# Performance work log

Measured on AMD Instinct MI355X. Metric: run time of the kernel, lower is better.

## Reference

```python
import jax, jax.numpy as jnp
import numpy as np

B, L, HID, NH, HD = 1, 2304, 3072, 24, 128
IMG = 2048
MLP = 4 * HID  # 12288
EPS = 1e-6


def _layernorm(x):
    mu = jnp.mean(x, axis=-1, keepdims=True)
    var = jnp.mean(jnp.square(x - mu), axis=-1, keepdims=True)
    return (x - mu) * jax.lax.rsqrt(var + EPS)


def _rmsnorm(x, w):
    ms = jnp.mean(jnp.square(x), axis=-1, keepdims=True)
    return x * jax.lax.rsqrt(ms + EPS) * w


def _rope_interleaved(x, cos, sin):
    # x: [B, S, H, D]; cos/sin: [1, S, 1, D] with pairwise-equal values (mode=1, GPT-J)
    x1 = x[..., 0::2]
    x2 = x[..., 1::2]
    c = cos[..., 0::2]
    s = sin[..., 0::2]
    even = x1 * c - x2 * s
    odd = x1 * s + x2 * c
    return jnp.stack([even, odd], axis=-1).reshape(x.shape)


def setup_inputs() -> dict:
    key = jax.random.key(0)
    ks = jax.random.split(key, 10)
    scale_in = 1.0 / np.sqrt(HID)
    x = jax.random.normal(ks[0], (B, L, HID), jnp.float32)
    vec = jax.random.normal(ks[1], (B, HID), jnp.float32)
    # RoPE tables (interleaved layout: value repeated per pair)
    pos = jnp.arange(IMG, dtype=jnp.float32)
    inv_freq = 1.0 / (10000.0 ** (jnp.arange(HD // 2, dtype=jnp.float32) / (HD // 2)))
    ang = pos[:, None] * inv_freq[None, :]               # [IMG, HD/2]
    freqs_cos = jnp.repeat(jnp.cos(ang), 2, axis=-1).reshape(1, IMG, 1, HD)
    freqs_sin = jnp.repeat(jnp.sin(ang), 2, axis=-1).reshape(1, IMG, 1, HD)
    mod_w = jax.random.normal(ks[2], (HID, 3 * HID), jnp.float32) * scale_in
    mod_b = jnp.zeros((3 * HID,), jnp.float32)
    w1 = jax.random.normal(ks[3], (HID, 3 * HID + MLP), jnp.float32) * scale_in
    b1 = jnp.zeros((3 * HID + MLP,), jnp.float32)
    q_norm_w = jnp.ones((HD,), jnp.float32)
    k_norm_w = jnp.ones((HD,), jnp.float32)
    w2 = jax.random.normal(ks[4], (HID + MLP, HID), jnp.float32) * (1.0 / np.sqrt(HID + MLP))
    b2 = jnp.zeros((HID,), jnp.float32)
    return {
        'x': x, 'vec': vec, 'img_len': IMG,
        'freqs_cos': freqs_cos, 'freqs_sin': freqs_sin,
        'mod_w': mod_w, 'mod_b': mod_b, 'w1': w1, 'b1': b1,
        'q_norm_w': q_norm_w, 'k_norm_w': k_norm_w, 'w2': w2, 'b2': b2,
    }


def reference(x, vec, img_len, freqs_cos, freqs_sin, mod_w, mod_b, w1, b1,
              q_norm_w, k_norm_w, w2, b2):
    # modulation: SiLU(vec) -> Linear -> shift/scale/gate  [B, HID] each
    mod = jax.nn.silu(vec) @ mod_w + mod_b
    shift, scale, gate = jnp.split(mod, 3, axis=-1)
    x_mod = _layernorm(x) * (1.0 + scale[:, None, :]) + shift[:, None, :]

    # fused QKV + MLP projection
    proj = x_mod @ w1 + b1                                  # [B, L, 3*HID + MLP]
    qkv, mlp = proj[..., :3 * HID], proj[..., 3 * HID:]
    q, k, v = [t[:, :, 0] for t in [None]] if False else None, None, None
    qkv = qkv.reshape(B, L, 3, NH, HD)
    q, k, v = qkv[:, :, 0], qkv[:, :, 1], qkv[:, :, 2]      # [B, L, NH, HD]

    q = _rmsnorm(q, q_norm_w)
    k = _rmsnorm(k, k_norm_w)

    # RoPE only on image tokens
    q = jnp.concatenate([_rope_interleaved(q[:, :img_len], freqs_cos, freqs_sin), q[:, img_len:]], axis=1)
    k = jnp.concatenate([_rope_interleaved(k[:, :img_len], freqs_cos, freqs_sin), k[:, img_len:]], axis=1)

    # full (img+txt) bidirectional attention
    attn_scale = 1.0 / np.sqrt(HD)
    scores = jnp.einsum('blhd,bmhd->bhlm', q, k) * attn_scale
    probs = jax.nn.softmax(scores, axis=-1)
    attn = jnp.einsum('bhlm,bmhd->blhd', probs, v).reshape(B, L, NH * HD)

    # output fusion: [attn | gelu_tanh(mlp)] @ w2
    out = jnp.concatenate([attn, jax.nn.gelu(mlp, approximate=True)], axis=-1) @ w2 + b2
    return x + out * gate[:, None, :]
```

## Files before the change

### kernel.cpp

```cpp
#include <hip/hip_runtime.h>

#define L_SEQ 2304
#define HID_D 3072
#define NH_D 24
#define HD_D 128
#define N1_D 21504
#define QKVN 9216
#define K2_D 15360
#define EPS_V 1e-6f
#define ATTN_SC 0.08838834764831843f

typedef __bf16 bf16x8 __attribute__((ext_vector_type(8)));
typedef float f32x4 __attribute__((ext_vector_type(4)));
typedef unsigned int u32x4 __attribute__((ext_vector_type(4)));
typedef unsigned short u16x8 __attribute__((ext_vector_type(8)));
typedef unsigned short u16x4 __attribute__((ext_vector_type(4)));

#define WAITVM(N) asm volatile("s_waitcnt vmcnt(" #N ")" ::: "memory")
#define LGKM0 asm volatile("s_waitcnt lgkmcnt(0)" ::: "memory")
#define SB0 __builtin_amdgcn_sched_barrier(0)

__device__ __forceinline__ unsigned short f2bf(float f) {
  unsigned int u = __builtin_bit_cast(unsigned int, f);
  u += 0x7fffu + ((u >> 16) & 1u);
  return (unsigned short)(u >> 16);
}

__device__ __forceinline__ float gelu_f(float x) {
  float u = 0.7978845608028654f * (x + 0.044715f * x * x * x);
  float e = __expf(2.f * u);
  float th = 1.f - 2.f / (e + 1.f);
  return 0.5f * x * (1.f + th);
}

__device__ __forceinline__ void gload16(const void* g, void* l) {
  __builtin_amdgcn_global_load_lds(
      (const __attribute__((address_space(1))) unsigned int*)g,
      (__attribute__((address_space(3))) unsigned int*)l, 16, 0, 0);
}

__global__ __launch_bounds__(256) void mod_partial_kernel(
    const float* __restrict__ vec, const float* __restrict__ mod_w,
    float* __restrict__ partial) {
  __shared__ float s[384];
  const int t = threadIdx.x;
  const int kb = blockIdx.y;
  const int k0 = kb * 384;
  for (int p = t; p < 384; p += 256) {
    float v = vec[k0 + p];
    s[p] = v / (1.f + __expf(-v));
  }
  __syncthreads();
  const int n = blockIdx.x * 256 + t;
  float acc = 0.f;
  const float* wp = mod_w + (size_t)k0 * QKVN + n;
#pragma unroll 4
  for (int j = 0; j < 384; ++j) acc += s[j] * wp[(size_t)j * QKVN];
  partial[kb * QKVN + n] = acc;
}

__global__ __launch_bounds__(256) void mod_reduce_kernel(
    const float* __restrict__ partial, const float* __restrict__ mod_b,
    float* __restrict__ mod) {
  const int n = blockIdx.x * 256 + threadIdx.x;
  float acc = mod_b[n];
#pragma unroll
  for (int i = 0; i < 8; ++i) acc += partial[i * QKVN + n];
  mod[n] = acc;
}

__global__ __launch_bounds__(256) void ln_mod_kernel(
    const float* __restrict__ x, const float* __restrict__ mod,
    unsigned short* __restrict__ xmod) {
  const int row = blockIdx.x;
  const int t = threadIdx.x;
  const float* xr = x + (size_t)row * HID_D;
  float4 v[3];
  float sum = 0.f, sq = 0.f;
#pragma unroll
  for (int p = 0; p < 3; ++p) {
    v[p] = *(const float4*)&xr[p * 1024 + t * 4];
    sum += v[p].x + v[p].y + v[p].z + v[p].w;
    sq += v[p].x * v[p].x + v[p].y * v[p].y + v[p].z * v[p].z + v[p].w * v[p].w;
  }
#pragma unroll
  for (int o = 1; o < 64; o <<= 1) {
    sum += __shfl_xor(sum, o);
    sq += __shfl_xor(sq, o);
  }
  __shared__ float rs[8];
  const int w = t >> 6;
  if ((t & 63) == 0) { rs[w] = sum; rs[4 + w] = sq; }
  __syncthreads();
  sum = rs[0] + rs[1] + rs[2] + rs[3];
  sq = rs[4] + rs[5] + rs[6] + rs[7];
  const float mu = sum * (1.f / HID_D);
  const float var = sq * (1.f / HID_D) - mu * mu;
  const float rstd = rsqrtf(var + EPS_V);
#pragma unroll
  for (int p = 0; p < 3; ++p) {
    const int c = p * 1024 + t * 4;
    float4 sc = *(const float4*)&mod[3072 + c];
    float4 sh = *(const float4*)&mod[c];
    u16x4 o4;
    o4[0] = f2bf((v[p].x - mu) * rstd * (1.f + sc.x) + sh.x);
    o4[1] = f2bf((v[p].y - mu) * rstd * (1.f + sc.y) + sh.y);
    o4[2] = f2bf((v[p].z - mu) * rstd * (1.f + sc.z) + sh.z);
    o4[3] = f2bf((v[p].w - mu) * rstd * (1.f + sc.w) + sh.w);
    *(u16x4*)&xmod[(size_t)row * HID_D + c] = o4;
  }
}

__global__ __launch_bounds__(256) void convert_transpose_kernel(
    const float* __restrict__ src, unsigned short* __restrict__ dst,
    const int K, const int N) {
  __shared__ unsigned short lt[64][72];
  const int t = threadIdx.x;
  const int n0 = blockIdx.x * 64;
  const int k0 = blockIdx.y * 64;
  const int kr = t >> 4;
  const int n4 = (t & 15) * 4;
#pragma unroll
  for (int p = 0; p < 4; ++p) {
    const int k = kr + p * 16;
    float4 v = *(const float4*)&src[(size_t)(k0 + k) * N + n0 + n4];
    lt[n4 + 0][k] = f2bf(v.x);
    lt[n4 + 1][k] = f2bf(v.y);
    lt[n4 + 2][k] = f2bf(v.z);
    lt[n4 + 3][k] = f2bf(v.w);
  }
  __syncthreads();
  const int nr = t >> 2;
  const int kc = (t & 3) * 16;
  u16x8 a = *(const u16x8*)&lt[nr][kc];
  u16x8 b = *(const u16x8*)&lt[nr][kc + 8];
  unsigned short* dp = &dst[(size_t)(n0 + nr) * K + k0 + kc];
  *(u16x8*)dp = a;
  *(u16x8*)(dp + 8) = b;
}

template <int BM>
__device__ __forceinline__ void gemm8_core(
    const unsigned short* __restrict__ A, const int lda,
    const unsigned short* __restrict__ B, const int ldb,
    const int m0, const int n0, const int nit, char* lds, f32x4 (*acc)[4]) {
  constexpr int AREG = (BM == 256) ? 16384 : 8192;
  constexpr int ABUF = 2 * AREG;
  constexpr int BOFF = 2 * ABUF;
  constexpr int BREG = 16384;
  constexpr int BBUF = 32768;
  constexpr int AROWS = (BM == 256) ? 128 : 64;
  constexpr int AI = (BM == 256) ? 2 : 1;
  constexpr int MF = (BM == 256) ? 4 : 2;
  constexpr int QM = (BM == 256) ? 64 : 32;

  const int t = threadIdx.x;
  const int lane = t & 63;
  const int w = t >> 6;
  const int g = lane >> 4;
  const int c = lane & 15;
  const int sr8 = lane >> 3;
  const int scol = ((lane & 7) ^ sr8) * 8;
  const int arg = w >> 2;
  const int brg = (w & 3) >> 1;
  const int bbase = (w & 1) * 64;

  auto stageA = [&](int buf, int rg, int kt) {
#pragma unroll
    for (int i = 0; i < AI; ++i)
      gload16(A + (size_t)(m0 + rg * AROWS + i * 64 + w * 8 + sr8) * lda +
                  kt * 64 + scol,
              lds + buf * ABUF + rg * AREG + i * 8192 + w * 1024);
  };
  auto stageB = [&](int buf, int rg, int kt) {
#pragma unroll
    for (int i = 0; i < 2; ++i)
      gload16(B + (size_t)(n0 + rg * 128 + i * 64 + w * 8 + sr8) * ldb +
                  kt * 64 + scol,
              lds + BOFF + buf * BBUF + rg * BREG + i * 8192 + w * 1024);
  };

  bf16x8 af[2 * MF], bq0[4], bq1[4];
  auto ldA = [&](int buf, int qm) {
    const char* ab = lds + buf * ABUF + arg * AREG;
#pragma unroll
    for (int i = 0; i < MF; ++i) {
      const int lr = qm * QM + i * 16 + c;
#pragma unroll
      for (int kk = 0; kk < 2; ++kk)
        af[i * 2 + kk] =
            *(const bf16x8*)(ab + lr * 128 + (((kk * 4 + g) ^ (c & 7)) << 4));
    }
  };
  auto ldB = [&](int buf, int qn, bf16x8* bq) {
    const char* bb = lds + BOFF + buf * BBUF + brg * BREG;
#pragma unroll
    for (int i = 0; i < 2; ++i) {
      const int lr = bbase + qn * 32 + i * 16 + c;
#pragma unroll
      for (int kk = 0; kk < 2; ++kk)
        bq[i * 2 + kk] =
            *(const bf16x8*)(bb + lr * 128 + (((kk * 4 + g) ^ (c & 7)) << 4));
    }
  };
  auto domf = [&](int qm, int qn, const bf16x8* bq) {
#pragma unroll
    for (int i = 0; i < MF; ++i)
#pragma unroll
      for (int n = 0; n < 2; ++n)
#pragma unroll
        for (int kk = 0; kk < 2; ++kk)
          acc[qm * MF + i][qn * 2 + n] = __builtin_amdgcn_mfma_f32_16x16x32_bf16(
              af[i * 2 + kk], bq[n * 2 + kk], acc[qm * MF + i][qn * 2 + n], 0, 0, 0);
  };
  auto MID = [&] {
    SB0;
    __builtin_amdgcn_s_barrier();
    LGKM0;
    SB0;
    __builtin_amdgcn_s_setprio(1);
  };
  auto END = [&] {
    __builtin_amdgcn_s_setprio(0);
    SB0;
    __builtin_amdgcn_s_barrier();
  };

  stageB(0, 0, 0); stageA(0, 0, 0); stageB(0, 1, 0); stageA(0, 1, 0);
  stageB(1, 0, 1); stageA(1, 0, 1);
  if constexpr (BM == 256) WAITVM(4); else WAITVM(3);
  __builtin_amdgcn_s_barrier();

  for (int j = 0; j < nit; ++j) {
    const int ta = 2 * j;
    const bool nl = (j + 1 < nit);
    ldA(0, 0); ldB(0, 0, bq0);
    stageB(1, 1, ta + 1);
    MID(); domf(0, 0, bq0); END();
    ldB(0, 1, bq1);
    stageA(1, 1, ta + 1);
    MID(); domf(0, 1, bq1); END();
    ldA(0, 1);
    if (nl) stageB(0, 0, ta + 2);
    MID(); domf(1, 1, bq1); END();
    if (nl) stageA(0, 0, ta + 2);
    MID(); domf(1, 0, bq0);
    __builtin_amdgcn_s_setprio(0); SB0;
    if (nl) { if constexpr (BM == 256) WAITVM(4); else WAITVM(3); }
    else WAITVM(0);
    __builtin_amdgcn_s_barrier();
    ldA(1, 0); ldB(1, 0, bq0);
    if (nl) stageB(0, 1, ta + 2);
    MID(); domf(0, 0, bq0); END();
    ldB(1, 1, bq1);
    if (nl) stageA(0, 1, ta + 2);
    MID(); domf(0, 1, bq1); END();
    ldA(1, 1);
    if (nl) stageB(1, 0, ta + 3);
    MID(); domf(1, 1, bq1); END();
    if (nl) stageA(1, 0, ta + 3);
    MID(); domf(1, 0, bq0);
    __builtin_amdgcn_s_setprio(0); SB0;
    if (nl) { if constexpr (BM == 256) WAITVM(4); else WAITVM(3); }
    __builtin_amdgcn_s_barrier();
  }
}

__global__ __launch_bounds__(512, 2) void gemm1_kernel(
    const unsigned short* __restrict__ xmod, const unsigned short* __restrict__ w1t,
    const float* __restrict__ b1, float* __restrict__ qkv,
    unsigned short* __restrict__ hbuf) {
  __shared__ __align__(16) char smem[131072];
  f32x4 acc[8][4];
  const f32x4 zero = {0.f, 0.f, 0.f, 0.f};
#pragma unroll
  for (int i = 0; i < 8; ++i)
#pragma unroll
    for (int j = 0; j < 4; ++j) acc[i][j] = zero;
  const int orig = blockIdx.x;
  const int xcd = orig & 7;
  const int wgid = (xcd < 4 ? xcd * 95 : 380 + (xcd - 4) * 94) + (orig >> 3);
  const int m0 = (wgid % 9) * 256;
  const int n0 = (wgid / 9) * 256;
  gemm8_core<256>(xmod, HID_D, w1t, HID_D, m0, n0, 24, smem, acc);
  const int lane = threadIdx.x & 63;
  const int g = lane >> 4, c = lane & 15;
  const int w = threadIdx.x >> 6;
  const int wm = (w >> 2) * 128, wn = (w & 3) * 64;
  const bool is_mlp = (n0 >= QKVN);
#pragma unroll
  for (int mf = 0; mf < 8; ++mf)
#pragma unroll
    for (int nf = 0; nf < 4; ++nf)
#pragma unroll
      for (int j = 0; j < 4; ++j) {
        const int row = m0 + wm + mf * 16 + g * 4 + j;
        const int col = n0 + wn + nf * 16 + c;
        const float v = acc[mf][nf][j] + b1[col];
        if (!is_mlp) {
          qkv[(size_t)row * QKVN + col] = v;
        } else {
          hbuf[(size_t)row * K2_D + HID_D + (col - QKVN)] = f2bf(gelu_f(v));
        }
      }
}

__global__ __launch_bounds__(512, 2) void gemm2_kernel(
    const unsigned short* __restrict__ hbuf, const unsigned short* __restrict__ w2t,
    const float* __restrict__ b2, const float* __restrict__ x,
    const float* __restrict__ mod, float* __restrict__ out) {
  __shared__ __align__(16) char smem[98304];
  f32x4 acc[4][4];
  const f32x4 zero = {0.f, 0.f, 0.f, 0.f};
#pragma unroll
  for (int i = 0; i < 4; ++i)
#pragma unroll
    for (int j = 0; j < 4; ++j) acc[i][j] = zero;
  const int orig = blockIdx.x;
  const int wgid = (orig & 7) * 27 + (orig >> 3);
  const int m0 = (wgid % 18) * 128;
  const int n0 = (wgid / 18) * 256;
  gemm8_core<128>(hbuf, K2_D, w2t, K2_D, m0, n0, 120, smem, acc);
  const int lane = threadIdx.x & 63;
  const int g = lane >> 4, c = lane & 15;
  const int w = threadIdx.x >> 6;
  const int wm = (w >> 2) * 64, wn = (w & 3) * 64;
#pragma unroll
  for (int mf = 0; mf < 4; ++mf)
#pragma unroll
    for (int nf = 0; nf < 4; ++nf)
#pragma unroll
      for (int j = 0; j < 4; ++j) {
        const int row = m0 + wm + mf * 16 + g * 4 + j;
        const int col = n0 + wn + nf * 16 + c;
        const float v = acc[mf][nf][j] + b2[col];
        out[(size_t)row * HID_D + col] =
            x[(size_t)row * HID_D + col] + v * mod[6144 + col];
      }
}

__global__ __launch_bounds__(256) void qk_norm_rope_kernel(
    const float* __restrict__ qkv, const float* __restrict__ qw,
    const float* __restrict__ kw, const float* __restrict__ fc,
    const float* __restrict__ fs, const int* __restrict__ img_len_p,
    unsigned short* __restrict__ qr, unsigned short* __restrict__ kr) {
  const int l = blockIdx.x;
  const int t = threadIdx.x;
  const int wv = t >> 6;
  const int lane = t & 63;
  const int img = *img_len_p;
  const bool do_rope = (l < img);
  float cc = 1.f, ss = 0.f;
  if (do_rope) {
    cc = fc[l * HD_D + 2 * lane];
    ss = fs[l * HD_D + 2 * lane];
  }
  const float qw0 = qw[2 * lane], qw1 = qw[2 * lane + 1];
  const float kw0 = kw[2 * lane], kw1 = kw[2 * lane + 1];
#pragma unroll
  for (int hh = 0; hh < 6; ++hh) {
    const int h = hh * 4 + wv;
    {
      float2 q2 = *(const float2*)&qkv[(size_t)l * QKVN + h * HD_D + 2 * lane];
      float sq = q2.x * q2.x + q2.y * q2.y;
#pragma unroll
      for (int o = 1; o < 64; o <<= 1) sq += __shfl_xor(sq, o);
      const float r = rsqrtf(sq * (1.f / HD_D) + EPS_V);
      float a = q2.x * r * qw0, b = q2.y * r * qw1;
      float e = a, od = b;
      if (do_rope) { e = a * cc - b * ss; od = a * ss + b * cc; }
      e *= ATTN_SC; od *= ATTN_SC;
      unsigned int pk = (unsigned)f2bf(e) | ((unsigned)f2bf(od) << 16);
      *(unsigned int*)&qr[((size_t)h * L_SEQ + l) * HD_D + 2 * lane] = pk;
    }
    {
      float2 k2 = *(const float2*)&qkv[(size_t)l * QKVN + HID_D + h * HD_D + 2 * lane];
      float sq = k2.x * k2.x + k2.y * k2.y;
#pragma unroll
      for (int o = 1; o < 64; o <<= 1) sq += __shfl_xor(sq, o);
      const float r = rsqrtf(sq * (1.f / HD_D) + EPS_V);
      float a = k2.x * r * kw0, b = k2.y * r * kw1;
      float e = a, od = b;
      if (do_rope) { e = a * cc - b * ss; od = a * ss + b * cc; }
      unsigned int pk = (unsigned)f2bf(e) | ((unsigned)f2bf(od) << 16);
      *(unsigned int*)&kr[((size_t)h * L_SEQ + l) * HD_D + 2 * lane] = pk;
    }
  }
}

__global__ __launch_bounds__(256) void v_transpose_kernel(
    const float* __restrict__ qkv, unsigned short* __restrict__ vT) {
  __shared__ unsigned short lv[128 * 64];
  const int h = blockIdx.y;
  const int l0 = blockIdx.x * 64;
  const int t = threadIdx.x;
#pragma unroll
  for (int p = 0; p < 8; ++p) {
    const int idx = p * 256 + t;
    const int l = idx >> 5;
    const int d4 = (idx & 31) * 4;
    float4 v = *(const float4*)&qkv[(size_t)(l0 + l) * QKVN + 2 * HID_D + h * HD_D + d4];
    const unsigned sw = (unsigned)(((d4 >> 2) & 7) << 4);
    *(unsigned short*)((char*)lv + (((d4 + 0) * 128 + 2 * l) ^ sw)) = f2bf(v.x);
    *(unsigned short*)((char*)lv + (((d4 + 1) * 128 + 2 * l) ^ sw)) = f2bf(v.y);
    *(unsigned short*)((char*)lv + (((d4 + 2) * 128 + 2 * l) ^ sw)) = f2bf(v.z);
    *(unsigned short*)((char*)lv + (((d4 + 3) * 128 + 2 * l) ^ sw)) = f2bf(v.w);
  }
  __syncthreads();
  const int d = t >> 1;
  const int half = t & 1;
  const unsigned swr = (unsigned)(((d >> 2) & 7) << 4);
#pragma unroll
  for (int j2 = 0; j2 < 4; ++j2) {
    u32x4 v = *(const u32x4*)((const char*)lv + ((d * 128 + half * 64 + j2 * 16) ^ swr));
    *(u32x4*)&vT[(size_t)(h * HD_D + d) * L_SEQ + l0 + half * 32 + j2 * 8] = v;
  }
}

__global__ __launch_bounds__(256) void attn_kernel(
    const unsigned short* __restrict__ qr, const unsigned short* __restrict__ kr,
    const unsigned short* __restrict__ vT, unsigned short* __restrict__ hbuf) {
  __shared__ unsigned short lds_k[64 * 128];
  __shared__ unsigned short lds_v[128 * 64];
  __shared__ unsigned short lds_p[4 * 16 * 64];
  const int hidx = blockIdx.y;
  const int l0 = blockIdx.x * 64;
  const int t = threadIdx.x;
  const int lane = t & 63;
  const int w = t >> 6;
  const int g = lane >> 4;
  const int c = lane & 15;

  bf16x8 qa[4];
  {
    const unsigned short* qrow = qr + ((size_t)hidx * L_SEQ + l0 + w * 16 + c) * HD_D;
#pragma unroll
    for (int ks = 0; ks < 4; ++ks)
      qa[ks] = *(const bf16x8*)&qrow[ks * 32 + g * 8];
  }
  f32x4 acc[8];
  const f32x4 zero = {0.f, 0.f, 0.f, 0.f};
#pragma unroll
  for (int i = 0; i < 8; ++i) acc[i] = zero;
  float m_r[4] = {-1e30f, -1e30f, -1e30f, -1e30f};
  float l_r[4] = {0.f, 0.f, 0.f, 0.f};

  for (int kv0 = 0; kv0 < L_SEQ; kv0 += 64) {
    __syncthreads();
#pragma unroll
    for (int p = 0; p < 4; ++p) {
      const int idx = p * 256 + t;
      const int r = idx >> 4, ch = idx & 15;
      u32x4 v = *(const u32x4*)&kr[((size_t)hidx * L_SEQ + kv0 + r) * HD_D + ch * 8];
      *(u32x4*)((char*)lds_k + ((r * 256 + ch * 16) ^ ((r & 7) << 4))) = v;
    }
#pragma unroll
    for (int p = 0; p < 4; ++p) {
      const int idx = p * 256 + t;
      const int d_ = idx >> 3, ch = idx & 7;
      u32x4 v = *(const u32x4*)&vT[(size_t)(hidx * HD_D + d_) * L_SEQ + kv0 + ch * 8];
      *(u32x4*)((char*)lds_v + ((d_ * 128 + ch * 16) ^ ((d_ & 7) << 4))) = v;
    }
    __syncthreads();
    f32x4 s[4];
#pragma unroll
    for (int cf = 0; cf < 4; ++cf) s[cf] = zero;
#pragma unroll
    for (int ks = 0; ks < 4; ++ks) {
      const int kb = (ks * 32 + g * 8) * 2;
#pragma unroll
      for (int cf = 0; cf < 4; ++cf) {
        const int kvr = cf * 16 + c;
        bf16x8 kf = *(const bf16x8*)((const char*)lds_k + ((kvr * 256 + kb) ^ ((kvr & 7) << 4)));
        s[cf] = __builtin_amdgcn_mfma_f32_16x16x32_bf16(qa[ks], kf, s[cf], 0, 0, 0);
      }
    }
    float pv[4][4];
    float alpha[4];
#pragma unroll
    for (int r = 0; r < 4; ++r) {
      float mx = fmaxf(fmaxf(s[0][r], s[1][r]), fmaxf(s[2][r], s[3][r]));
      mx = fmaxf(mx, __shfl_xor(mx, 1));
      mx = fmaxf(mx, __shfl_xor(mx, 2));
      mx = fmaxf(mx, __shfl_xor(mx, 4));
      mx = fmaxf(mx, __shfl_xor(mx, 8));
      const float mnew = fmaxf(m_r[r], mx);
      alpha[r] = __expf(m_r[r] - mnew);
      float rsum = 0.f;
#pragma unroll
      for (int cf = 0; cf < 4; ++cf) {
        const float p_ = __expf(s[cf][r] - mnew);
        pv[cf][r] = p_;
        rsum += p_;
      }
      rsum += __shfl_xor(rsum, 1);
      rsum += __shfl_xor(rsum, 2);
      rsum += __shfl_xor(rsum, 4);
      rsum += __shfl_xor(rsum, 8);
      l_r[r] = l_r[r] * alpha[r] + rsum;
      m_r[r] = mnew;
    }
#pragma unroll
    for (int of = 0; of < 8; ++of)
#pragma unroll
      for (int r = 0; r < 4; ++r) acc[of][r] *= alpha[r];
#pragma unroll
    for (int cf = 0; cf < 4; ++cf)
#pragma unroll
      for (int r = 0; r < 4; ++r) {
        const int row = g * 4 + r;
        const int col = cf * 16 + c;
        *(unsigned short*)((char*)lds_p +
                           ((w * 2048 + row * 128 + col * 2) ^ ((row & 7) << 4))) =
            f2bf(pv[cf][r]);
      }
    asm volatile("s_waitcnt lgkmcnt(0)" ::: "memory");
    __builtin_amdgcn_sched_barrier(0);
#pragma unroll
    for (int ks = 0; ks < 2; ++ks) {
      bf16x8 pa = *(const bf16x8*)((const char*)lds_p +
                                   ((w * 2048 + c * 128 + (ks * 32 + g * 8) * 2) ^
                                    ((c & 7) << 4)));
#pragma unroll
      for (int of = 0; of < 8; ++of) {
        const int dcol = of * 16 + c;
        bf16x8 vb = *(const bf16x8*)((const char*)lds_v +
                                     ((dcol * 128 + (ks * 32 + g * 8) * 2) ^
                                      ((dcol & 7) << 4)));
        acc[of] = __builtin_amdgcn_mfma_f32_16x16x32_bf16(pa, vb, acc[of], 0, 0, 0);
      }
    }
  }
#pragma unroll
  for (int of = 0; of < 8; ++of)
#pragma unroll
    for (int r = 0; r < 4; ++r) {
      const int row = l0 + w * 16 + g * 4 + r;
      const int col = hidx * HD_D + of * 16 + c;
      hbuf[(size_t)row * K2_D + col] = f2bf(acc[of][r] / l_r[r]);
    }
}

extern "C" void kernel_launch(void* const* d_in, const int* in_sizes, int n_in,
                              void* d_out, int out_size, void* d_ws, size_t ws_size,
                              hipStream_t stream) {
  (void)in_sizes; (void)n_in; (void)out_size; (void)ws_size;
  const float* x = (const float*)d_in[0];
  const float* vec = (const float*)d_in[1];
  const int* img_len = (const int*)d_in[2];
  const float* fc = (const float*)d_in[3];
  const float* fs = (const float*)d_in[4];
  const float* mod_w = (const float*)d_in[5];
  const float* mod_b = (const float*)d_in[6];
  const float* w1 = (const float*)d_in[7];
  const float* b1 = (const float*)d_in[8];
  const float* qw = (const float*)d_in[9];
  const float* kw = (const float*)d_in[10];
  const float* w2 = (const float*)d_in[11];
  const float* b2 = (const float*)d_in[12];
  float* out = (float*)d_out;

  char* wsb = (char*)d_ws;
  float* mod = (float*)(wsb + 0);
  float* partial = (float*)(wsb + 36864);
  unsigned short* xmod = (unsigned short*)(wsb + 331776);
  float* qkv = (float*)(wsb + 14487552);
  unsigned short* hbuf = (unsigned short*)(wsb + 99422208);
  unsigned short* qr = (unsigned short*)(wsb + 170201088);
  unsigned short* kr = (unsigned short*)(wsb + 184356864);
  unsigned short* vT = (unsigned short*)(wsb + 198512640);
  unsigned short* wt = (unsigned short*)(wsb + 212668416);

  mod_partial_kernel<<<dim3(36, 8), 256, 0, stream>>>(vec, mod_w, partial);
  mod_reduce_kernel<<<36, 256, 0, stream>>>(partial, mod_b, mod);
  ln_mod_kernel<<<2304, 256, 0, stream>>>(x, mod, xmod);
  convert_transpose_kernel<<<dim3(N1_D / 64, HID_D / 64), 256, 0, stream>>>(
      w1, wt, HID_D, N1_D);
  gemm1_kernel<<<756, 512, 0, stream>>>(xmod, wt, b1, qkv, hbuf);
  convert_transpose_kernel<<<dim3(HID_D / 64, K2_D / 64), 256, 0, stream>>>(
      w2, wt, K2_D, HID_D);
  qk_norm_rope_kernel<<<2304, 256, 0, stream>>>(qkv, qw, kw, fc, fs, img_len, qr, kr);
  v_transpose_kernel<<<dim3(36, 24), 256, 0, stream>>>(qkv, vT);
  attn_kernel<<<dim3(36, 24), 256, 0, stream>>>(qr, kr, vT, hbuf);
  gemm2_kernel<<<216, 512, 0, stream>>>(hbuf, wt, b2, x, mod, out);
}
```

Measured before the change: 935.7 us.

## Store QKV intermediate as bf16 and triple-buffer the second GEMM pipeline

The fp32 QKV buffer written by the first GEMM is replaced with bf16, which halves its write and read traffic in the QK-norm/RoPE and V-transpose kernels. The second GEMM switches from a double-buffered core to a new three-stage LDS pipeline (144KB shared memory, 80 iterations of three k-tiles) so that more global loads are in flight during MFMA work. The pipeline adds LDS pressure, which may lower occupancy. Rounding Q/K/V to bf16 before the norm adds a small precision loss.

```diff
diff --git a/kernel.cpp b/kernel.cpp
--- a/kernel.cpp
+++ b/kernel.cpp
@@ -24,6 +24,9 @@
   unsigned int u = __builtin_bit_cast(unsigned int, f);
   u += 0x7fffu + ((u >> 16) & 1u);
   return (unsigned short)(u >> 16);
+}
+__device__ __forceinline__ float bf2f(unsigned short u) {
+  return __builtin_bit_cast(float, (unsigned int)u << 16);
 }
 
 __device__ __forceinline__ float gelu_f(float x) {
@@ -266,9 +269,124 @@
   }
 }
 
+__device__ __forceinline__ void gemm6_core(
+    const unsigned short* __restrict__ A, const int lda,
+    const unsigned short* __restrict__ B, const int ldb,
+    const int m0, const int n0, const int nit3, char* lds, f32x4 (*acc)[4]) {
+  const int t = threadIdx.x;
+  const int lane = t & 63;
+  const int w = t >> 6;
+  const int g = lane >> 4;
+  const int c = lane & 15;
+  const int sr8 = lane >> 3;
+  const int scol = ((lane & 7) ^ sr8) * 8;
+  const int arg = w >> 2;
+  const int brg = (w & 3) >> 1;
+  const int bbase = (w & 1) * 64;
+
+  auto stageA = [&](int buf, int kt) {
+#pragma unroll
+    for (int rg = 0; rg < 2; ++rg)
+      gload16(A + (size_t)(m0 + rg * 64 + w * 8 + sr8) * lda + kt * 64 + scol,
+              lds + buf * 16384 + rg * 8192 + w * 1024);
+  };
+  auto stageB = [&](int buf, int rg, int kt) {
+#pragma unroll
+    for (int i = 0; i < 2; ++i)
+      gload16(B + (size_t)(n0 + rg * 128 + i * 64 + w * 8 + sr8) * ldb +
+                  kt * 64 + scol,
+              lds + 49152 + buf * 32768 + rg * 16384 + i * 8192 + w * 1024);
+  };
+
+  bf16x8 af[8], bq[8];
+  auto ldA = [&](int buf) {
+    const char* ab = lds + buf * 16384 + arg * 8192;
+#pragma unroll
+    for (int i = 0; i < 4; ++i) {
+      const int lr = i * 16 + c;
+#pragma unroll
+      for (int kk = 0; kk < 2; ++kk)
+        af[i * 2 + kk] =
+            *(const bf16x8*)(ab + lr * 128 + (((kk * 4 + g) ^ (c & 7)) << 4));
+    }
+  };
+  auto ldB = [&](int buf, int half) {
+    const char* bb = lds + 49152 + buf * 32768 + brg * 16384;
+#pragma unroll
+    for (int i = 0; i < 2; ++i) {
+      const int lr = bbase + (half * 2 + i) * 16 + c;
+#pragma unroll
+      for (int kk = 0; kk < 2; ++kk)
+        bq[half * 4 + i * 2 + kk] =
+            *(const bf16x8*)(bb + lr * 128 + (((kk * 4 + g) ^ (c & 7)) << 4));
+    }
+  };
+  auto domf = [&](int half) {
+#pragma unroll
+    for (int i = 0; i < 4; ++i)
+#pragma unroll
+      for (int n = 0; n < 2; ++n)
+#pragma unroll
+        for (int kk = 0; kk < 2; ++kk)
+          acc[i][half * 2 + n] = __builtin_amdgcn_mfma_f32_16x16x32_bf16(
+              af[i * 2 + kk], bq[half * 4 + n * 2 + kk], acc[i][half * 2 + n],
+              0, 0, 0);
+  };
+  auto MID = [&] {
+    SB0;
+    __builtin_amdgcn_s_barrier();
+    LGKM0;
+    SB0;
+    __builtin_amdgcn_s_setprio(1);
+  };
+  auto END = [&] {
+    __builtin_amdgcn_s_setprio(0);
+    SB0;
+    __builtin_amdgcn_s_barrier();
+  };
+
+  stageA(0, 0); stageB(0, 0, 0); stageB(0, 1, 0);
+  stageA(1, 1); stageB(1, 0, 1); stageB(1, 1, 1);
+  stageA(2, 2);
+  WAITVM(8);
+  __builtin_amdgcn_s_barrier();
+
+  for (int j = 0; j < nit3; ++j) {
+    const int T = 3 * j;
+    const bool nl = (j + 1 < nit3);
+    ldA(0); ldB(0, 0);
+    stageB(2, 0, T + 2); stageB(2, 1, T + 2);
+    MID(); domf(0); END();
+    ldB(0, 1);
+    if (nl) stageA(0, T + 3);
+    MID(); domf(1);
+    __builtin_amdgcn_s_setprio(0); SB0;
+    if (nl) WAITVM(8); else WAITVM(6);
+    __builtin_amdgcn_s_barrier();
+    ldA(1); ldB(1, 0);
+    if (nl) stageB(0, 0, T + 3);
+    MID(); domf(0); END();
+    ldB(1, 1);
+    if (nl) { stageB(0, 1, T + 3); stageA(1, T + 4); }
+    MID(); domf(1);
+    __builtin_amdgcn_s_setprio(0); SB0;
+    if (nl) WAITVM(8); else WAITVM(0);
+    __builtin_amdgcn_s_barrier();
+    ldA(2); ldB(2, 0);
+    if (nl) { stageB(1, 0, T + 4); stageB(1, 1, T + 4); }
+    MID(); domf(0); END();
+    ldB(2, 1);
+    if (nl) stageA(2, T + 5);
+    MID(); domf(1);
+    __builtin_amdgcn_s_setprio(0); SB0;
+    if (nl) WAITVM(8);
+    __builtin_amdgcn_s_barrier();
+  }
+}
+
 __global__ __launch_bounds__(512, 2) void gemm1_kernel(
     const unsigned short* __restrict__ xmod, const unsigned short* __restrict__ w1t,
-    const float* __restrict__ b1, float* __restrict__ qkv,
+    const float* __restrict__ b1, unsigned short* __restrict__ qkv,
     unsigned short* __restrict__ hbuf) {
   __shared__ __align__(16) char smem[131072];
   f32x4 acc[8][4];
@@ -298,7 +416,7 @@
         const int col = n0 + wn + nf * 16 + c;
         const float v = acc[mf][nf][j] + b1[col];
         if (!is_mlp) {
-          qkv[(size_t)row * QKVN + col] = v;
+          qkv[(size_t)row * QKVN + col] = f2bf(v);
         } else {
           hbuf[(size_t)row * K2_D + HID_D + (col - QKVN)] = f2bf(gelu_f(v));
         }
@@ -309,7 +427,7 @@
     const unsigned short* __restrict__ hbuf, const unsigned short* __restrict__ w2t,
     const float* __restrict__ b2, const float* __restrict__ x,
     const float* __restrict__ mod, float* __restrict__ out) {
-  __shared__ __align__(16) char smem[98304];
+  __shared__ __align__(16) char smem[147456];
   f32x4 acc[4][4];
   const f32x4 zero = {0.f, 0.f, 0.f, 0.f};
 #pragma unroll
@@ -320,7 +438,7 @@
   const int wgid = (orig & 7) * 27 + (orig >> 3);
   const int m0 = (wgid % 18) * 128;
   const int n0 = (wgid / 18) * 256;
-  gemm8_core<128>(hbuf, K2_D, w2t, K2_D, m0, n0, 120, smem, acc);
+  gemm6_core(hbuf, K2_D, w2t, K2_D, m0, n0, 80, smem, acc);
   const int lane = threadIdx.x & 63;
   const int g = lane >> 4, c = lane & 15;
   const int w = threadIdx.x >> 6;
@@ -340,7 +458,7 @@
 }
 
 __global__ __launch_bounds__(256) void qk_norm_rope_kernel(
-    const float* __restrict__ qkv, const float* __restrict__ qw,
+    const unsigned short* __restrict__ qkv, const float* __restrict__ qw,
     const float* __restrict__ kw, const float* __restrict__ fc,
     const float* __restrict__ fs, const int* __restrict__ img_len_p,
     unsigned short* __restrict__ qr, unsigned short* __restrict__ kr) {
@@ -361,12 +479,14 @@
   for (int hh = 0; hh < 6; ++hh) {
     const int h = hh * 4 + wv;
     {
-      float2 q2 = *(const float2*)&qkv[(size_t)l * QKVN + h * HD_D + 2 * lane];
-      float sq = q2.x * q2.x + q2.y * q2.y;
+      unsigned int pq = *(const unsigned int*)&qkv[(size_t)l * QKVN + h * HD_D + 2 * lane];
+      float q0 = bf2f((unsigned short)(pq & 0xffff));
+      float q1 = bf2f((unsigned short)(pq >> 16));
+      float sq = q0 * q0 + q1 * q1;
 #pragma unroll
       for (int o = 1; o < 64; o <<= 1) sq += __shfl_xor(sq, o);
       const float r = rsqrtf(sq * (1.f / HD_D) + EPS_V);
-      float a = q2.x * r * qw0, b = q2.y * r * qw1;
+      float a = q0 * r * qw0, b = q1 * r * qw1;
       float e = a, od = b;
       if (do_rope) { e = a * cc - b * ss; od = a * ss + b * cc; }
       e *= ATTN_SC; od *= ATTN_SC;
@@ -374,12 +494,14 @@
       *(unsigned int*)&qr[((size_t)h * L_SEQ + l) * HD_D + 2 * lane] = pk;
     }
     {
-      float2 k2 = *(const float2*)&qkv[(size_t)l * QKVN + HID_D + h * HD_D + 2 * lane];
-      float sq = k2.x * k2.x + k2.y * k2.y;
+      unsigned int pkk = *(const unsigned int*)&qkv[(size_t)l * QKVN + HID_D + h * HD_D + 2 * lane];
+      float k0 = bf2f((unsigned short)(pkk & 0xffff));
+      float k1 = bf2f((unsigned short)(pkk >> 16));
+      float sq = k0 * k0 + k1 * k1;
 #pragma unroll
       for (int o = 1; o < 64; o <<= 1) sq += __shfl_xor(sq, o);
       const float r = rsqrtf(sq * (1.f / HD_D) + EPS_V);
-      float a = k2.x * r * kw0, b = k2.y * r * kw1;
+      float a = k0 * r * kw0, b = k1 * r * kw1;
       float e = a, od = b;
       if (do_rope) { e = a * cc - b * ss; od = a * ss + b * cc; }
       unsigned int pk = (unsigned)f2bf(e) | ((unsigned)f2bf(od) << 16);
@@ -389,22 +511,23 @@
 }
 
 __global__ __launch_bounds__(256) void v_transpose_kernel(
-    const float* __restrict__ qkv, unsigned short* __restrict__ vT) {
+    const unsigned short* __restrict__ qkv, unsigned short* __restrict__ vT) {
   __shared__ unsigned short lv[128 * 64];
   const int h = blockIdx.y;
   const int l0 = blockIdx.x * 64;
   const int t = threadIdx.x;
 #pragma unroll
-  for (int p = 0; p < 8; ++p) {
+  for (int p = 0; p < 4; ++p) {
     const int idx = p * 256 + t;
-    const int l = idx >> 5;
-    const int d4 = (idx & 31) * 4;
-    float4 v = *(const float4*)&qkv[(size_t)(l0 + l) * QKVN + 2 * HID_D + h * HD_D + d4];
-    const unsigned sw = (unsigned)(((d4 >> 2) & 7) << 4);
-    *(unsigned short*)((char*)lv + (((d4 + 0) * 128 + 2 * l) ^ sw)) = f2bf(v.x);
-    *(unsigned short*)((char*)lv + (((d4 + 1) * 128 + 2 * l) ^ sw)) = f2bf(v.y);
-    *(unsigned short*)((char*)lv + (((d4 + 2) * 128 + 2 * l) ^ sw)) = f2bf(v.z);
-    *(unsigned short*)((char*)lv + (((d4 + 3) * 128 + 2 * l) ^ sw)) = f2bf(v.w);
+    const int l = idx >> 4;
+    const int d8 = (idx & 15) * 8;
+    u16x8 v = *(const u16x8*)&qkv[(size_t)(l0 + l) * QKVN + 2 * HID_D + h * HD_D + d8];
+#pragma unroll
+    for (int e = 0; e < 8; ++e) {
+      const int d = d8 + e;
+      const unsigned sw = (unsigned)(((d >> 2) & 7) << 4);
+      *(unsigned short*)((char*)lv + (((unsigned)d * 128 + 2 * l) ^ sw)) = v[e];
+    }
   }
   __syncthreads();
   const int d = t >> 1;
@@ -564,7 +687,7 @@
   float* mod = (float*)(wsb + 0);
   float* partial = (float*)(wsb + 36864);
   unsigned short* xmod = (unsigned short*)(wsb + 331776);
-  float* qkv = (float*)(wsb + 14487552);
+  unsigned short* qkv = (unsigned short*)(wsb + 14487552);
   unsigned short* hbuf = (unsigned short*)(wsb + 99422208);
   unsigned short* qr = (unsigned short*)(wsb + 170201088);
   unsigned short* kr = (unsigned short*)(wsb + 184356864);
```

Result: slower. 966.9 us (+3.3%).

## Store QKV intermediate in bf16 and register-prefetch next attention K/V tile

Applied to the files above, without the earlier changes.

The gemm1 epilogue now writes the QKV projection as bf16 instead of fp32, and the qk-norm/rope and V-transpose kernels read bf16, which halves that intermediate's write and read traffic. The attention kernel loads the next K/V tile into registers while the current tile is being computed, overlapping global loads with MFMA work at the cost of extra registers. The final normalization uses a reciprocal multiply instead of a divide. Rounding QKV to bf16 before the RMS norm adds a small amount of precision loss.

```diff
diff --git a/kernel.cpp b/kernel.cpp
--- a/kernel.cpp
+++ b/kernel.cpp
@@ -24,6 +24,9 @@
   unsigned int u = __builtin_bit_cast(unsigned int, f);
   u += 0x7fffu + ((u >> 16) & 1u);
   return (unsigned short)(u >> 16);
+}
+__device__ __forceinline__ float bf2f(unsigned short u) {
+  return __builtin_bit_cast(float, (unsigned int)u << 16);
 }
 
 __device__ __forceinline__ float gelu_f(float x) {
@@ -268,7 +271,7 @@
 
 __global__ __launch_bounds__(512, 2) void gemm1_kernel(
     const unsigned short* __restrict__ xmod, const unsigned short* __restrict__ w1t,
-    const float* __restrict__ b1, float* __restrict__ qkv,
+    const float* __restrict__ b1, unsigned short* __restrict__ qkv,
     unsigned short* __restrict__ hbuf) {
   __shared__ __align__(16) char smem[131072];
   f32x4 acc[8][4];
@@ -298,7 +301,7 @@
         const int col = n0 + wn + nf * 16 + c;
         const float v = acc[mf][nf][j] + b1[col];
         if (!is_mlp) {
-          qkv[(size_t)row * QKVN + col] = v;
+          qkv[(size_t)row * QKVN + col] = f2bf(v);
         } else {
           hbuf[(size_t)row * K2_D + HID_D + (col - QKVN)] = f2bf(gelu_f(v));
         }
@@ -340,7 +343,7 @@
 }
 
 __global__ __launch_bounds__(256) void qk_norm_rope_kernel(
-    const float* __restrict__ qkv, const float* __restrict__ qw,
+    const unsigned short* __restrict__ qkv, const float* __restrict__ qw,
     const float* __restrict__ kw, const float* __restrict__ fc,
     const float* __restrict__ fs, const int* __restrict__ img_len_p,
     unsigned short* __restrict__ qr, unsigned short* __restrict__ kr) {
@@ -361,12 +364,14 @@
   for (int hh = 0; hh < 6; ++hh) {
     const int h = hh * 4 + wv;
     {
-      float2 q2 = *(const float2*)&qkv[(size_t)l * QKVN + h * HD_D + 2 * lane];
-      float sq = q2.x * q2.x + q2.y * q2.y;
+      unsigned int pq = *(const unsigned int*)&qkv[(size_t)l * QKVN + h * HD_D + 2 * lane];
+      float q0 = bf2f((unsigned short)(pq & 0xffff));
+      float q1 = bf2f((unsigned short)(pq >> 16));
+      float sq = q0 * q0 + q1 * q1;
 #pragma unroll
       for (int o = 1; o < 64; o <<= 1) sq += __shfl_xor(sq, o);
       const float r = rsqrtf(sq * (1.f / HD_D) + EPS_V);
-      float a = q2.x * r * qw0, b = q2.y * r * qw1;
+      float a = q0 * r * qw0, b = q1 * r * qw1;
       float e = a, od = b;
       if (do_rope) { e = a * cc - b * ss; od = a * ss + b * cc; }
       e *= ATTN_SC; od *= ATTN_SC;
@@ -374,12 +379,14 @@
       *(unsigned int*)&qr[((size_t)h * L_SEQ + l) * HD_D + 2 * lane] = pk;
     }
     {
-      float2 k2 = *(const float2*)&qkv[(size_t)l * QKVN + HID_D + h * HD_D + 2 * lane];
-      float sq = k2.x * k2.x + k2.y * k2.y;
+      unsigned int pkk = *(const unsigned int*)&qkv[(size_t)l * QKVN + HID_D + h * HD_D + 2 * lane];
+      float k0 = bf2f((unsigned short)(pkk & 0xffff));
+      float k1 = bf2f((unsigned short)(pkk >> 16));
+      float sq = k0 * k0 + k1 * k1;
 #pragma unroll
       for (int o = 1; o < 64; o <<= 1) sq += __shfl_xor(sq, o);
       const float r = rsqrtf(sq * (1.f / HD_D) + EPS_V);
-      float a = k2.x * r * kw0, b = k2.y * r * kw1;
+      float a = k0 * r * kw0, b = k1 * r * kw1;
       float e = a, od = b;
       if (do_rope) { e = a * cc - b * ss; od = a * ss + b * cc; }
       unsigned int pk = (unsigned)f2bf(e) | ((unsigned)f2bf(od) << 16);
@@ -389,22 +396,23 @@
 }
 
 __global__ __launch_bounds__(256) void v_transpose_kernel(
-    const float* __restrict__ qkv, unsigned short* __restrict__ vT) {
+    const unsigned short* __restrict__ qkv, unsigned short* __restrict__ vT) {
   __shared__ unsigned short lv[128 * 64];
   const int h = blockIdx.y;
   const int l0 = blockIdx.x * 64;
   const int t = threadIdx.x;
 #pragma unroll
-  for (int p = 0; p < 8; ++p) {
+  for (int p = 0; p < 4; ++p) {
     const int idx = p * 256 + t;
-    const int l = idx >> 5;
-    const int d4 = (idx & 31) * 4;
-    float4 v = *(const float4*)&qkv[(size_t)(l0 + l) * QKVN + 2 * HID_D + h * HD_D + d4];
-    const unsigned sw = (unsigned)(((d4 >> 2) & 7) << 4);
-    *(unsigned short*)((char*)lv + (((d4 + 0) * 128 + 2 * l) ^ sw)) = f2bf(v.x);
-    *(unsigned short*)((char*)lv + (((d4 + 1) * 128 + 2 * l) ^ sw)) = f2bf(v.y);
-    *(unsigned short*)((char*)lv + (((d4 + 2) * 128 + 2 * l) ^ sw)) = f2bf(v.z);
-    *(unsigned short*)((char*)lv + (((d4 + 3) * 128 + 2 * l) ^ sw)) = f2bf(v.w);
+    const int l = idx >> 4;
+    const int d8 = (idx & 15) * 8;
+    u16x8 v = *(const u16x8*)&qkv[(size_t)(l0 + l) * QKVN + 2 * HID_D + h * HD_D + d8];
+#pragma unroll
+    for (int e = 0; e < 8; ++e) {
+      const int d = d8 + e;
+      const unsigned sw = (unsigned)(((d >> 2) & 7) << 4);
+      *(unsigned short*)((char*)lv + (((unsigned)d * 128 + 2 * l) ^ sw)) = v[e];
+    }
   }
   __syncthreads();
   const int d = t >> 1;
@@ -445,23 +453,39 @@
   float m_r[4] = {-1e30f, -1e30f, -1e30f, -1e30f};
   float l_r[4] = {0.f, 0.f, 0.f, 0.f};
 
-  for (int kv0 = 0; kv0 < L_SEQ; kv0 += 64) {
-    __syncthreads();
+  u32x4 kreg[4], vreg[4];
+  auto load_tile = [&](int kv0) {
 #pragma unroll
     for (int p = 0; p < 4; ++p) {
       const int idx = p * 256 + t;
       const int r = idx >> 4, ch = idx & 15;
-      u32x4 v = *(const u32x4*)&kr[((size_t)hidx * L_SEQ + kv0 + r) * HD_D + ch * 8];
-      *(u32x4*)((char*)lds_k + ((r * 256 + ch * 16) ^ ((r & 7) << 4))) = v;
+      kreg[p] = *(const u32x4*)&kr[((size_t)hidx * L_SEQ + kv0 + r) * HD_D + ch * 8];
     }
 #pragma unroll
     for (int p = 0; p < 4; ++p) {
       const int idx = p * 256 + t;
       const int d_ = idx >> 3, ch = idx & 7;
-      u32x4 v = *(const u32x4*)&vT[(size_t)(hidx * HD_D + d_) * L_SEQ + kv0 + ch * 8];
-      *(u32x4*)((char*)lds_v + ((d_ * 128 + ch * 16) ^ ((d_ & 7) << 4))) = v;
-    }
+      vreg[p] = *(const u32x4*)&vT[(size_t)(hidx * HD_D + d_) * L_SEQ + kv0 + ch * 8];
+    }
+  };
+  load_tile(0);
+
+  for (int kv0 = 0; kv0 < L_SEQ; kv0 += 64) {
     __syncthreads();
+#pragma unroll
+    for (int p = 0; p < 4; ++p) {
+      const int idx = p * 256 + t;
+      const int r = idx >> 4, ch = idx & 15;
+      *(u32x4*)((char*)lds_k + ((r * 256 + ch * 16) ^ ((r & 7) << 4))) = kreg[p];
+    }
+#pragma unroll
+    for (int p = 0; p < 4; ++p) {
+      const int idx = p * 256 + t;
+      const int d_ = idx >> 3, ch = idx & 7;
+      *(u32x4*)((char*)lds_v + ((d_ * 128 + ch * 16) ^ ((d_ & 7) << 4))) = vreg[p];
+    }
+    __syncthreads();
+    if (kv0 + 64 < L_SEQ) load_tile(kv0 + 64);
     f32x4 s[4];
 #pragma unroll
     for (int cf = 0; cf < 4; ++cf) s[cf] = zero;
@@ -531,13 +555,16 @@
       }
     }
   }
+  float rinv[4];
+#pragma unroll
+  for (int r = 0; r < 4; ++r) rinv[r] = 1.f / l_r[r];
 #pragma unroll
   for (int of = 0; of < 8; ++of)
 #pragma unroll
     for (int r = 0; r < 4; ++r) {
       const int row = l0 + w * 16 + g * 4 + r;
       const int col = hidx * HD_D + of * 16 + c;
-      hbuf[(size_t)row * K2_D + col] = f2bf(acc[of][r] / l_r[r]);
+      hbuf[(size_t)row * K2_D + col] = f2bf(acc[of][r] * rinv[r]);
     }
 }
 
@@ -564,7 +591,7 @@
   float* mod = (float*)(wsb + 0);
   float* partial = (float*)(wsb + 36864);
   unsigned short* xmod = (unsigned short*)(wsb + 331776);
-  float* qkv = (float*)(wsb + 14487552);
+  unsigned short* qkv = (unsigned short*)(wsb + 14487552);
   unsigned short* hbuf = (unsigned short*)(wsb + 99422208);
   unsigned short* qr = (unsigned short*)(wsb + 170201088);
   unsigned short* kr = (unsigned short*)(wsb + 184356864);
```

New measurement: 957.3 us. 1.02x slower.
